# Performance work log

Measured on AMD Instinct MI355X. Metric: run time of the kernel, lower is better.

## Reference

```python
import jax, jax.numpy as jnp
import numpy as np

B, S, DIM = 2, 2048, 2048
H, HKV = 16, 8
HD = DIM // H          # 128
N_REP = H // HKV       # 2
EPS = 1e-6


def rmsnorm(x, w):
    return x * jax.lax.rsqrt(jnp.mean(x * x, axis=-1, keepdims=True) + EPS) * w


def apply_rope(x, cis):
    # x: [b, s, h, hd]; cis: [b, s, hd//2, 2] (cos, sin)
    xr = x.reshape(*x.shape[:-1], HD // 2, 2)
    x_re, x_im = xr[..., 0], xr[..., 1]
    c_re = cis[..., 0][:, :, None, :]  # broadcast over heads
    c_im = cis[..., 1][:, :, None, :]
    o_re = x_re * c_re - x_im * c_im
    o_im = x_re * c_im + x_im * c_re
    return jnp.stack([o_re, o_im], axis=-1).reshape(x.shape)


def setup_inputs() -> dict:
    key = jax.random.key(0)
    k1, k2, k3 = jax.random.split(key, 3)
    x = jax.random.normal(k1, (B, S, DIM), dtype=jnp.float32)
    x_mask = jnp.ones((B, S), dtype=bool)
    # rotary freqs: standard 10000-base, precomputed as (cos, sin)
    inv_freq = 1.0 / (10000.0 ** (jnp.arange(0, HD, 2, dtype=jnp.float32) / HD))
    ang = jnp.arange(S, dtype=jnp.float32)[:, None] * inv_freq[None, :]  # [s, hd//2]
    cis = jnp.stack([jnp.cos(ang), jnp.sin(ang)], axis=-1)               # [s, hd//2, 2]
    freqs_cis = jnp.broadcast_to(cis[None], (B, S, HD // 2, 2))
    scale = 1.0 / np.sqrt(DIM)
    w_qkv = jax.random.normal(k2, ((H + 2 * HKV) * HD, DIM), dtype=jnp.float32) * scale
    w_out = jax.random.normal(k3, (DIM, H * HD), dtype=jnp.float32) * scale
    q_norm_w = jnp.ones((HD,), dtype=jnp.float32)
    k_norm_w = jnp.ones((HD,), dtype=jnp.float32)
    return {"x": x, "x_mask": x_mask, "freqs_cis": freqs_cis,
            "w_qkv": w_qkv, "w_out": w_out,
            "q_norm_w": q_norm_w, "k_norm_w": k_norm_w}


def reference(x, x_mask, freqs_cis, w_qkv, w_out, q_norm_w, k_norm_w):
    bsz, seqlen, _ = x.shape
    qkv = x @ w_qkv.T                                   # [b, s, (H+2*HKV)*HD]
    xq, xk, xv = jnp.split(qkv, [H * HD, (H + HKV) * HD], axis=-1)
    xq = xq.reshape(bsz, seqlen, H, HD)
    xk = xk.reshape(bsz, seqlen, HKV, HD)
    xv = xv.reshape(bsz, seqlen, HKV, HD)
    xq = rmsnorm(xq, q_norm_w)
    xk = rmsnorm(xk, k_norm_w)
    xq = apply_rope(xq, freqs_cis)
    xk = apply_rope(xk, freqs_cis)
    # GQA: repeat kv heads (torch: unsqueeze/repeat/flatten)
    xk = jnp.repeat(xk, N_REP, axis=2)                  # [b, s, H, HD]
    xv = jnp.repeat(xv, N_REP, axis=2)
    softmax_scale = 1.0 / np.sqrt(HD)
    scores = jnp.einsum('bqhd,bkhd->bhqk', xq, xk) * softmax_scale
    scores = jnp.where(x_mask[:, None, None, :], scores, jnp.float32(-1e9))
    attn = jax.nn.softmax(scores, axis=-1)
    out = jnp.einsum('bhqk,bkhd->bqhd', attn, xv)       # [b, s, H, HD]
    out = out.reshape(bsz, seqlen, H * HD)
    return out @ w_out.T
```

## Files before the change

kernel.cpp:

```cpp
#include <hip/hip_runtime.h>


typedef __attribute__((ext_vector_type(8))) short short8;
typedef __attribute__((ext_vector_type(8))) unsigned short ushort8;
typedef __attribute__((ext_vector_type(4))) float f32x4;
typedef __attribute__((ext_vector_type(16))) float f32x16;

__device__ __forceinline__ unsigned short to_bf16(float f) {
  union { float f; unsigned u; } v; v.f = f;
  unsigned r = v.u + 0x7fffu + ((v.u >> 16) & 1u);
  return (unsigned short)(r >> 16);
}
__device__ __forceinline__ float bfhi_f32(unsigned u) {
  union { unsigned u; float f; } v; v.u = u & 0xffff0000u; return v.f;
}
__device__ __forceinline__ float bflo_f32(unsigned u) {
  union { unsigned u; float f; } v; v.u = u << 16; return v.f;
}

#define GLOAD16(gp, lp) __builtin_amdgcn_global_load_lds(                      \
    (const __attribute__((address_space(1))) void*)(gp),                       \
    (__attribute__((address_space(3))) void*)(lp), 16, 0, 0)

__global__ __launch_bounds__(256) void cvt3_bf16_k(const float* __restrict__ s0,
                                                   const float* __restrict__ s1,
                                                   const float* __restrict__ s2,
                                                   unsigned short* __restrict__ d0,
                                                   unsigned short* __restrict__ d1,
                                                   unsigned short* __restrict__ d2) {
  int i = blockIdx.x * 256 + threadIdx.x;
  const float* sp; unsigned short* dp;
  if (i < 1048576)      { sp = s0; dp = d0; }
  else if (i < 2097152) { sp = s1; dp = d1; i -= 1048576; }
  else                  { sp = s2; dp = d2; i -= 2097152; }
  const float4* v = (const float4*)sp + (size_t)i * 2;
  float4 a = v[0], b = v[1];
  ushort8 t;
  t[0] = to_bf16(a.x); t[1] = to_bf16(a.y); t[2] = to_bf16(a.z); t[3] = to_bf16(a.w);
  t[4] = to_bf16(b.x); t[5] = to_bf16(b.y); t[6] = to_bf16(b.z); t[7] = to_bf16(b.w);
  *((ushort8*)dp + i) = t;
}

#define SWZ(r, cb) ((cb) ^ (((r) & 7) << 4))

#define VMW_STEADY() do {                                                      \
    if constexpr (BM == 256) asm volatile("s_waitcnt vmcnt(6)" ::: "memory");  \
    else                     asm volatile("s_waitcnt vmcnt(5)" ::: "memory");  \
  } while (0)

#define STAGE_HALF(sb, sm, sh, skt) do {                                       \
    const char* gb_ = (sm) ? gB : gA;                                          \
    char* lb_ = ldsAB + (sb) * BUFSTR +                                        \
                ((sm) ? 2 * AH + (sh) * 16384 : (sh) * AH);                    \
    const int rows_ = (sm) ? 128 : (BM >> 1);                                  \
    const int nld_ = (sm) ? 2 : (BM >> 7);                                     \
    _Pragma("unroll")                                                          \
    for (int j_ = 0; j_ < nld_; ++j_) {                                        \
      const int c_ = tid + j_ * 512;                                           \
      const int rl_ = c_ >> 3, u_ = c_ & 7;                                    \
      GLOAD16(gb_ + (size_t)((sh) * rows_ + rl_) * rstr + (size_t)(skt) * 128  \
                  + SWZ(rl_, u_ * 16),                                         \
              lb_ + j_ * 8192 + wv * 1024);                                    \
    }                                                                          \
  } while (0)

#define GPHASE(bb, qd, sb, sm, sh, skt, DOVM) do {                             \
    _Pragma("unroll")                                                          \
    for (int i_ = 0; i_ < FPP; ++i_) {                                         \
      _Pragma("unroll")                                                        \
      for (int ks_ = 0; ks_ < 2; ++ks_) {                                      \
        const int ar_ = ((qd) * FPP + i_) * 16 + r15;                          \
        af[i_][ks_] = *(const short8*)(ldsAB + (bb) * BUFSTR + wr * AH         \
                        + ar_ * 128 + SWZ(ar_, ks_ * 64 + g4 * 16));           \
      }                                                                        \
    }                                                                          \
    if ((qd) == 0) {                                                           \
      _Pragma("unroll")                                                        \
      for (int ni_ = 0; ni_ < 4; ++ni_)                                        \
        _Pragma("unroll")                                                      \
        for (int ks_ = 0; ks_ < 2; ++ks_) {                                    \
          const int br_ = (wc & 1) * 64 + ni_ * 16 + r15;                      \
          bf[ni_][ks_] = *(const short8*)(ldsAB + (bb) * BUFSTR + 2 * AH       \
                           + (wc >> 1) * 16384 + br_ * 128                     \
                           + SWZ(br_, ks_ * 64 + g4 * 16));                    \
        }                                                                      \
    }                                                                          \
    asm volatile("s_waitcnt lgkmcnt(0)" ::: "memory");                         \
    __builtin_amdgcn_sched_barrier(0);                                         \
    STAGE_HALF(sb, sm, sh, skt);                                               \
    __builtin_amdgcn_s_barrier();                                              \
    __builtin_amdgcn_s_setprio(1);                                             \
    _Pragma("unroll")                                                          \
    for (int ni_ = 0; ni_ < 4; ++ni_)                                          \
      _Pragma("unroll")                                                        \
      for (int i_ = 0; i_ < FPP; ++i_)                                         \
        _Pragma("unroll")                                                      \
        for (int ks_ = 0; ks_ < 2; ++ks_)                                      \
          acc[(qd) * FPP + i_][ni_] = __builtin_amdgcn_mfma_f32_16x16x32_bf16( \
              af[i_][ks_], bf[ni_][ks_], acc[(qd) * FPP + i_][ni_], 0, 0, 0);  \
    __builtin_amdgcn_s_setprio(0);                                             \
    if (DOVM) VMW_STEADY();                                                    \
    __builtin_amdgcn_s_barrier();                                              \
  } while (0)

template <int BM, typename OT>
__global__ __launch_bounds__(512, 2) void gemm8p_k(const unsigned short* __restrict__ A,
                                                   const unsigned short* __restrict__ B,
                                                   OT* __restrict__ C,
                                                   int M, int N, int K) {
  constexpr int AH = BM * 64;
  constexpr int BUFSTR = 2 * AH + 32768;
  constexpr int FPP = BM / 128;
  constexpr int MFR = BM / 32;
  __shared__ __align__(16) char ldsAB[2 * BUFSTR];
  const int tid = threadIdx.x, lane = tid & 63, wv = tid >> 6;
  const int wr = wv >> 2, wc = wv & 3;
  const int r15 = lane & 15, g4 = lane >> 4;
  const int gx = gridDim.x, nwg = gx * gridDim.y;
  int bid = blockIdx.y * gx + blockIdx.x;
  bid = (bid & 7) * (nwg >> 3) + (bid >> 3);
  const int m0 = (bid / gx) * BM, n0 = (bid % gx) << 8;
  const char* gA = (const char*)(A + (size_t)m0 * K);
  const char* gB = (const char*)(B + (size_t)n0 * K);
  const size_t rstr = (size_t)K * 2;
  const int KT = K >> 6, NIT = KT >> 1;

  f32x4 acc[MFR][4];
  #pragma unroll
  for (int mi = 0; mi < MFR; ++mi)
    #pragma unroll
    for (int ni = 0; ni < 4; ++ni) acc[mi][ni] = (f32x4){0.f, 0.f, 0.f, 0.f};
  short8 af[2][2], bf[4][2];

  STAGE_HALF(0, 1, 0, 0); STAGE_HALF(0, 1, 1, 0);
  STAGE_HALF(0, 0, 0, 0); STAGE_HALF(0, 0, 1, 0);
  STAGE_HALF(1, 1, 0, 1); STAGE_HALF(1, 1, 1, 1);
  STAGE_HALF(1, 0, 0, 1);
  VMW_STEADY();
  __builtin_amdgcn_s_barrier();

  for (int it = 0; it < NIT; ++it) {
    const int kt1c = 2 * it + 1;
    int ktn0 = 2 * it + 2; if (ktn0 > KT - 1) ktn0 = KT - 1;
    int ktn1 = 2 * it + 3; if (ktn1 > KT - 1) ktn1 = KT - 1;
    GPHASE(0, 0, 1, 0, 1, kt1c, 0);
    GPHASE(0, 1, 0, 1, 0, ktn0, 0);
    GPHASE(0, 2, 0, 1, 1, ktn0, 0);
    GPHASE(0, 3, 0, 0, 0, ktn0, 1);
    GPHASE(1, 0, 0, 0, 1, ktn0, 0);
    GPHASE(1, 1, 1, 1, 0, ktn1, 0);
    GPHASE(1, 2, 1, 1, 1, ktn1, 0);
    GPHASE(1, 3, 1, 0, 0, ktn1, 1);
  }
  asm volatile("s_waitcnt vmcnt(0)" ::: "memory");

  const int crow = m0 + wr * (BM >> 1), ccol = n0 + wc * 64;
  #pragma unroll
  for (int mi = 0; mi < MFR; ++mi)
    #pragma unroll
    for (int ni = 0; ni < 4; ++ni)
      #pragma unroll
      for (int r = 0; r < 4; ++r) {
        const size_t idx = (size_t)(crow + mi * 16 + g4 * 4 + r) * N
                         + (ccol + ni * 16 + r15);
        if constexpr (sizeof(OT) == 4) C[idx] = acc[mi][ni][r];
        else                           C[idx] = to_bf16(acc[mi][ni][r]);
      }
}

__global__ __launch_bounds__(256) void rmsrope_k(const unsigned short* __restrict__ qkv,
                                                 const float* __restrict__ freqs,
                                                 const float* __restrict__ qw,
                                                 const float* __restrict__ kw,
                                                 unsigned short* __restrict__ Qg,
                                                 unsigned short* __restrict__ Kg) {
  const int row = blockIdx.x;
  const int b = row >> 11, s = row & 2047;
  const int lane = threadIdx.x & 63, wave = threadIdx.x >> 6;
  const unsigned short* base = qkv + (size_t)row * 4096;
  const float2 cs = ((const float2*)(freqs + (size_t)row * 128))[lane];
  const int tile = s >> 6, kv = s & 63;
  for (int hh = wave; hh < 24; hh += 4) {
    const bool isq = hh < 16;
    const unsigned u = *(const unsigned*)(base + hh * 128 + 2 * lane);
    const float xre = bflo_f32(u), xim = bfhi_f32(u);
    float ssq = xre * xre + xim * xim;
    #pragma unroll
    for (int m = 1; m <= 32; m <<= 1) ssq += __shfl_xor(ssq, m);
    const float rs = rsqrtf(ssq * (1.0f / 128.0f) + 1e-6f);
    const float sscale = isq ? 0.12751743f : 1.0f;
    const float* wp = isq ? qw : kw;
    const float xr = xre * rs * wp[2 * lane];
    const float xi = xim * rs * wp[2 * lane + 1];
    const float o_re = (xr * cs.x - xi * cs.y) * sscale;
    const float o_im = (xr * cs.y + xi * cs.x) * sscale;
    unsigned pk = (unsigned)to_bf16(o_re) | ((unsigned)to_bf16(o_im) << 16);
    if (isq) {
      *(unsigned*)(Qg + ((size_t)(b * 16 + hh) * 2048 + s) * 128 + 2 * lane) = pk;
    } else {
      const int kvh = b * 8 + (hh - 16);
      const size_t off = ((size_t)(kvh * 32 + tile) * 16 + (lane >> 2)) * 1024
                       + kv * 16 + (lane & 3) * 4;
      *(unsigned*)((char*)Kg + off) = pk;
    }
  }
}

__global__ __launch_bounds__(128) void transpose_v_k(const unsigned short* __restrict__ qkv,
                                                     unsigned short* __restrict__ Vt) {
  const int sc = blockIdx.x, bh = blockIdx.y;
  const int b = bh >> 3, d = threadIdx.x, s0 = sc << 6;
  const unsigned short* src = qkv + (size_t)(b * 2048 + s0) * 4096
                              + (3072 + (bh & 7) * 128 + d);
  char* dstT = (char*)Vt + (size_t)(bh * 32 + sc) * 16384;
  for (int j0 = 0; j0 < 64; j0 += 8) {
    ushort8 t;
    #pragma unroll
    for (int j = 0; j < 8; ++j) t[j] = src[(size_t)(j0 + j) * 4096];
    *(ushort8*)(dstT + (((j0 >> 3) * 128 + d) << 4)) = t;
  }
}

__global__ __launch_bounds__(512, 1) void attn32_k(const unsigned short* __restrict__ Qg,
                                                   const unsigned short* __restrict__ Kg,
                                                   const unsigned short* __restrict__ Vt,
                                                   unsigned short* __restrict__ Og) {
  __shared__ __align__(16) unsigned short Ks[3][64 * 128];
  __shared__ __align__(16) unsigned short Vs[3][128 * 64];
  const int tid = threadIdx.x, lane = tid & 63, wv = tid >> 6;
  const int l31 = lane & 31, hi = lane >> 5;
  const int bh = blockIdx.y, b = bh >> 4, h = bh & 15;
  const int kvh = b * 8 + (h >> 1);
  const int qw = (blockIdx.x << 8) + wv * 32;
  const char* Qbase = (const char*)(Qg + ((size_t)bh * 2048 + qw) * 128);
  const char* Kbase = (const char*)Kg + (size_t)kvh * 524288;
  const char* Vbase = (const char*)Vt + (size_t)kvh * 524288;
  const int kox = hi * 1024 + l31 * 16;
  const int vox = hi * 2048 + l31 * 16;

  short8 qf[8];
  #pragma unroll
  for (int kk = 0; kk < 8; ++kk)
    qf[kk] = *(const short8*)(Qbase + l31 * 256 + kk * 32 + hi * 16);

  f32x16 oa[4];
  #pragma unroll
  for (int d = 0; d < 4; ++d)
    #pragma unroll
    for (int r = 0; r < 16; ++r) oa[d][r] = 0.f;
  float m2 = 0.f, lrun = 0.f;

#define STAGE_KV(tt, bb) do {                                                  \
    const char* ks_ = Kbase + (size_t)(tt) * 16384;                            \
    const char* vs_ = Vbase + (size_t)(tt) * 16384;                            \
    _Pragma("unroll")                                                          \
    for (int i_ = 0; i_ < 2; ++i_) {                                           \
      const int c_ = (i_ * 512 + tid) << 4;                                    \
      GLOAD16(ks_ + c_, (char*)Ks[bb] + c_);                                   \
      GLOAD16(vs_ + c_, (char*)Vs[bb] + c_);                                   \
    }                                                                          \
  } while (0)

  STAGE_KV(0, 0);
  STAGE_KV(1, 1);
  asm volatile("s_waitcnt vmcnt(4)" ::: "memory");
  __builtin_amdgcn_sched_barrier(0);
  __builtin_amdgcn_s_barrier();
  __builtin_amdgcn_sched_barrier(0);

  int c0 = 0, c1 = 1, c2 = 2;
  for (int t = 0; t < 32; ++t) {
    if (t < 30) STAGE_KV(t + 2, c2);
    const char* KsB = (const char*)Ks[0] + c0 * 16384;
    const char* VsB = (const char*)Vs[0] + c0 * 16384;

    f32x16 sc[2];
    #pragma unroll
    for (int c = 0; c < 2; ++c)
      #pragma unroll
      for (int r = 0; r < 16; ++r) sc[c][r] = 0.f;
    __builtin_amdgcn_s_setprio(1);
    #pragma unroll
    for (int kk = 0; kk < 8; ++kk) {
      #pragma unroll
      for (int c = 0; c < 2; ++c) {
        short8 kf = *(const short8*)(KsB + kk * 2048 + c * 512 + kox);
        sc[c] = __builtin_amdgcn_mfma_f32_32x32x16_bf16(kf, qf[kk], sc[c], 0, 0, 0);
      }
    }
    __builtin_amdgcn_s_setprio(0);

    float p0[16], p1[16];
    #pragma unroll
    for (int r = 0; r < 16; ++r) p0[r] = __builtin_amdgcn_exp2f(sc[0][r] - m2);
    #pragma unroll
    for (int r = 0; r < 16; ++r) p1[r] = __builtin_amdgcn_exp2f(sc[1][r] - m2);
    float tm[8];
    #pragma unroll
    for (int r = 0; r < 8; ++r)
      tm[r] = fmaxf(fmaxf(p0[r], p0[r + 8]), fmaxf(p1[r], p1[r + 8]));
    #pragma unroll
    for (int s = 4; s; s >>= 1)
      #pragma unroll
      for (int r = 0; r < s; ++r) tm[r] = fmaxf(tm[r], tm[r + s]);
    const float pmax = fmaxf(tm[0], __shfl_xor(tm[0], 32));
    if (!__all(pmax <= 256.f)) {
      float sm[8];
      #pragma unroll
      for (int r = 0; r < 8; ++r)
        sm[r] = fmaxf(fmaxf(sc[0][r], sc[0][r + 8]),
                      fmaxf(sc[1][r], sc[1][r + 8]));
      #pragma unroll
      for (int s = 4; s; s >>= 1)
        #pragma unroll
        for (int r = 0; r < s; ++r) sm[r] = fmaxf(sm[r], sm[r + s]);
      float smax = fmaxf(sm[0], __shfl_xor(sm[0], 32));
      smax = fmaxf(smax, m2);
      const float al = __builtin_amdgcn_exp2f(m2 - smax);
      lrun *= al;
      #pragma unroll
      for (int r = 0; r < 16; ++r) {
        const int crr = (r & 3) + ((r >> 2) << 3) + (hi << 2);
        const float aq = __shfl(al, crr);
        #pragma unroll
        for (int d = 0; d < 4; ++d) oa[d][r] *= aq;
      }
      m2 = smax;
      #pragma unroll
      for (int r = 0; r < 16; ++r) p0[r] = __builtin_amdgcn_exp2f(sc[0][r] - m2);
      #pragma unroll
      for (int r = 0; r < 16; ++r) p1[r] = __builtin_amdgcn_exp2f(sc[1][r] - m2);
    }
    float ts[8];
    #pragma unroll
    for (int r = 0; r < 8; ++r)
      ts[r] = (p0[r] + p0[r + 8]) + (p1[r] + p1[r + 8]);
    #pragma unroll
    for (int s = 4; s; s >>= 1)
      #pragma unroll
      for (int r = 0; r < s; ++r) ts[r] += ts[r + s];
    lrun += ts[0];

    short8 pa[4];
    #pragma unroll
    for (int ks = 0; ks < 4; ++ks) {
      const int base = (ks & 1) << 3;
      const float* pp = (ks >> 1) ? p1 : p0;
      unsigned w0, w1, w2, w3;
      asm("v_cvt_pk_bf16_f32 %0, %1, %2" : "=v"(w0)
          : "v"(pp[base + 0]), "v"(pp[base + 1]));
      asm("v_cvt_pk_bf16_f32 %0, %1, %2" : "=v"(w1)
          : "v"(pp[base + 2]), "v"(pp[base + 3]));
      asm("v_cvt_pk_bf16_f32 %0, %1, %2" : "=v"(w2)
          : "v"(pp[base + 4]), "v"(pp[base + 5]));
      asm("v_cvt_pk_bf16_f32 %0, %1, %2" : "=v"(w3)
          : "v"(pp[base + 6]), "v"(pp[base + 7]));
      asm("v_permlane32_swap_b32 %0, %1" : "+v"(w0), "+v"(w2));
      asm("v_permlane32_swap_b32 %0, %1" : "+v"(w1), "+v"(w3));
      union { unsigned u[4]; short8 s8; } pu;
      pu.u[0] = w0; pu.u[1] = w1; pu.u[2] = w2; pu.u[3] = w3;
      pa[ks] = pu.s8;
    }

    __builtin_amdgcn_s_setprio(1);
    #pragma unroll
    for (int ks = 0; ks < 4; ++ks) {
      #pragma unroll
      for (int d = 0; d < 4; ++d) {
        short8 vf = *(const short8*)(VsB + ks * 4096 + d * 512 + vox);
        oa[d] = __builtin_amdgcn_mfma_f32_32x32x16_bf16(pa[ks], vf, oa[d], 0, 0, 0);
      }
    }
    __builtin_amdgcn_s_setprio(0);

    __builtin_amdgcn_sched_barrier(0);
    if (t < 30) asm volatile("s_waitcnt vmcnt(4)" ::: "memory");
    else        asm volatile("s_waitcnt vmcnt(0)" ::: "memory");
    asm volatile("s_waitcnt lgkmcnt(0)" ::: "memory");
    __builtin_amdgcn_sched_barrier(0);
    __builtin_amdgcn_s_barrier();
    __builtin_amdgcn_sched_barrier(0);
    { const int tp = c0; c0 = c1; c1 = c2; c2 = tp; }
  }

  const float lt = lrun + __shfl_xor(lrun, 32);
  const float inv = 1.f / lt;
  #pragma unroll
  for (int r = 0; r < 16; ++r) {
    const int crr = (r & 3) + ((r >> 2) << 3) + (hi << 2);
    const float iv = __shfl(inv, crr);
    const size_t rowoff = (size_t)(b * 2048 + qw + crr) * 2048 + h * 128;
    #pragma unroll
    for (int d = 0; d < 4; ++d)
      Og[rowoff + d * 32 + l31] = to_bf16(oa[d][r] * iv);
  }
}

extern "C" void kernel_launch(void* const* d_in, const int* in_sizes, int n_in,
                              void* d_out, int out_size, void* d_ws, size_t ws_size,
                              hipStream_t stream) {
  const float* x     = (const float*)d_in[0];
  const float* freqs = (const float*)d_in[2];
  const float* w_qkv = (const float*)d_in[3];
  const float* w_out = (const float*)d_in[4];
  const float* qnw   = (const float*)d_in[5];
  const float* knw   = (const float*)d_in[6];
  float* out = (float*)d_out;

  char* ws = (char*)d_ws;
  unsigned short* x_bf    = (unsigned short*)(ws);
  unsigned short* wqkv_bf = (unsigned short*)(ws + (16u << 20));
  unsigned short* wout_bf = (unsigned short*)(ws + (32u << 20));
  unsigned short* qkvb    = (unsigned short*)(ws + (40u << 20));
  unsigned short* Qg      = (unsigned short*)(ws + (104u << 20));
  unsigned short* Kg      = (unsigned short*)(ws + (120u << 20));
  unsigned short* Vt       = wqkv_bf;
  unsigned short* attn_out = x_bf;

  cvt3_bf16_k<<<10240, 256, 0, stream>>>(x, w_qkv, w_out, x_bf, wqkv_bf, wout_bf);
  gemm8p_k<256, unsigned short><<<dim3(16, 16), 512, 0, stream>>>(
      x_bf, wqkv_bf, qkvb, 4096, 4096, 2048);
  rmsrope_k<<<4096, 256, 0, stream>>>(qkvb, freqs, qnw, knw, Qg, Kg);
  transpose_v_k<<<dim3(32, 16), 128, 0, stream>>>(qkvb, Vt);
  attn32_k<<<dim3(8, 32), 512, 0, stream>>>(Qg, Kg, Vt, attn_out);
  gemm8p_k<128, float><<<dim3(8, 32), 512, 0, stream>>>(
      attn_out, wout_bf, out, 4096, 2048, 2048);
}
```

Baseline: 211.9 us.

## Process KV tiles in pairs with double buffering, halving barriers per pass

The attention loop now stages two 64-key KV tiles per iteration into a double-buffered LDS layout, replacing the triple-buffered single-tile ring. Each iteration runs both QK^T products up front, then softmax and PV for each tile in turn. This halves the number of block barriers and waits, and gives the scheduler more independent MFMA work. In exchange it prefetches only one pair ahead, drops the setprio hints, uses more LDS (128KB) and more registers, and the wait is now vmcnt(0) every iteration.

Result: faster. 207.0 us (-2.3%).

```diff
diff --git a/kernel.cpp b/kernel.cpp
--- a/kernel.cpp
+++ b/kernel.cpp
@@ -225,8 +225,8 @@
                                                    const unsigned short* __restrict__ Kg,
                                                    const unsigned short* __restrict__ Vt,
                                                    unsigned short* __restrict__ Og) {
-  __shared__ __align__(16) unsigned short Ks[3][64 * 128];
-  __shared__ __align__(16) unsigned short Vs[3][128 * 64];
+  __shared__ __align__(16) char KsL[2 * 32768];
+  __shared__ __align__(16) char VsL[2 * 32768];
   const int tid = threadIdx.x, lane = tid & 63, wv = tid >> 6;
   const int l31 = lane & 31, hi = lane >> 5;
   const int bh = blockIdx.y, b = bh >> 4, h = bh & 15;
@@ -250,137 +250,148 @@
     for (int r = 0; r < 16; ++r) oa[d][r] = 0.f;
   float m2 = 0.f, lrun = 0.f;
 
-#define STAGE_KV(tt, bb) do {                                                  \
-    const char* ks_ = Kbase + (size_t)(tt) * 16384;                            \
-    const char* vs_ = Vbase + (size_t)(tt) * 16384;                            \
+#define STAGE_PAIR(tp, pb) do {                                                \
+    const char* kp_ = Kbase + (size_t)(tp) * 32768;                            \
+    const char* vp_ = Vbase + (size_t)(tp) * 32768;                            \
     _Pragma("unroll")                                                          \
     for (int i_ = 0; i_ < 2; ++i_) {                                           \
       const int c_ = (i_ * 512 + tid) << 4;                                    \
-      GLOAD16(ks_ + c_, (char*)Ks[bb] + c_);                                   \
-      GLOAD16(vs_ + c_, (char*)Vs[bb] + c_);                                   \
-    }                                                                          \
-  } while (0)
-
-  STAGE_KV(0, 0);
-  STAGE_KV(1, 1);
-  asm volatile("s_waitcnt vmcnt(4)" ::: "memory");
+      GLOAD16(kp_ + c_,         KsL + (pb) * 32768 + c_);                      \
+      GLOAD16(kp_ + 16384 + c_, KsL + (pb) * 32768 + 16384 + c_);              \
+      GLOAD16(vp_ + c_,         VsL + (pb) * 32768 + c_);                      \
+      GLOAD16(vp_ + 16384 + c_, VsL + (pb) * 32768 + 16384 + c_);              \
+    }                                                                          \
+  } while (0)
+
+#define QK_TILE(scv, ksb) do {                                                 \
+    _Pragma("unroll")                                                          \
+    for (int c = 0; c < 2; ++c)                                                \
+      _Pragma("unroll")                                                        \
+      for (int r = 0; r < 16; ++r) scv[c][r] = 0.f;                            \
+    _Pragma("unroll")                                                          \
+    for (int kk = 0; kk < 8; ++kk) {                                           \
+      _Pragma("unroll")                                                        \
+      for (int c = 0; c < 2; ++c) {                                            \
+        short8 kf = *(const short8*)((ksb) + kk * 2048 + c * 512 + kox);       \
+        scv[c] = __builtin_amdgcn_mfma_f32_32x32x16_bf16(kf, qf[kk], scv[c],   \
+                                                         0, 0, 0);             \
+      }                                                                        \
+    }                                                                          \
+  } while (0)
+
+#define SM_TILE(scv, pp0, pp1) do {                                            \
+    _Pragma("unroll")                                                          \
+    for (int r = 0; r < 16; ++r) pp0[r] = __builtin_amdgcn_exp2f(scv[0][r] - m2); \
+    _Pragma("unroll")                                                          \
+    for (int r = 0; r < 16; ++r) pp1[r] = __builtin_amdgcn_exp2f(scv[1][r] - m2); \
+    float tm[8];                                                               \
+    _Pragma("unroll")                                                          \
+    for (int r = 0; r < 8; ++r)                                                \
+      tm[r] = fmaxf(fmaxf(pp0[r], pp0[r + 8]), fmaxf(pp1[r], pp1[r + 8]));     \
+    _Pragma("unroll")                                                          \
+    for (int s = 4; s; s >>= 1)                                                \
+      _Pragma("unroll")                                                        \
+      for (int r = 0; r < s; ++r) tm[r] = fmaxf(tm[r], tm[r + s]);             \
+    const float pmax = fmaxf(tm[0], __shfl_xor(tm[0], 32));                    \
+    if (!__all(pmax <= 256.f)) {                             \
+      float sm_[8];                                                            \
+      _Pragma("unroll")                                                        \
+      for (int r = 0; r < 8; ++r)                                              \
+        sm_[r] = fmaxf(fmaxf(scv[0][r], scv[0][r + 8]),                        \
+                       fmaxf(scv[1][r], scv[1][r + 8]));                       \
+      _Pragma("unroll")                                                        \
+      for (int s = 4; s; s >>= 1)                                              \
+        _Pragma("unroll")                                                      \
+        for (int r = 0; r < s; ++r) sm_[r] = fmaxf(sm_[r], sm_[r + s]);        \
+      float smax = fmaxf(sm_[0], __shfl_xor(sm_[0], 32));                      \
+      smax = fmaxf(smax, m2);                                                  \
+      const float al = __builtin_amdgcn_exp2f(m2 - smax);                      \
+      lrun *= al;                                                              \
+      _Pragma("unroll")                                                        \
+      for (int r = 0; r < 16; ++r) {                                           \
+        const int crr = (r & 3) + ((r >> 2) << 3) + (hi << 2);                 \
+        const float aq = __shfl(al, crr);                                      \
+        _Pragma("unroll")                                                      \
+        for (int d = 0; d < 4; ++d) oa[d][r] *= aq;                            \
+      }                                                                        \
+      m2 = smax;                                                               \
+      _Pragma("unroll")                                                        \
+      for (int r = 0; r < 16; ++r) pp0[r] = __builtin_amdgcn_exp2f(scv[0][r] - m2); \
+      _Pragma("unroll")                                                        \
+      for (int r = 0; r < 16; ++r) pp1[r] = __builtin_amdgcn_exp2f(scv[1][r] - m2); \
+    }                                                                          \
+    float ts[8];                                                               \
+    _Pragma("unroll")                                                          \
+    for (int r = 0; r < 8; ++r)                                                \
+      ts[r] = (pp0[r] + pp0[r + 8]) + (pp1[r] + pp1[r + 8]);                   \
+    _Pragma("unroll")                                                          \
+    for (int s = 4; s; s >>= 1)                                                \
+      _Pragma("unroll")                                                        \
+      for (int r = 0; r < s; ++r) ts[r] += ts[r + s];                          \
+    lrun += ts[0];                                                             \
+  } while (0)
+
+#define PV_TILE(pp0, pp1, vsb) do {                                            \
+    short8 pa[4];                                                              \
+    _Pragma("unroll")                                                          \
+    for (int ks = 0; ks < 4; ++ks) {                                           \
+      const int base = (ks & 1) << 3;                                          \
+      const float* pp = (ks >> 1) ? pp1 : pp0;                                 \
+      unsigned w0, w1, w2, w3;                                                 \
+      asm("v_cvt_pk_bf16_f32 %0, %1, %2" : "=v"(w0)                            \
+          : "v"(pp[base + 0]), "v"(pp[base + 1]));                             \
+      asm("v_cvt_pk_bf16_f32 %0, %1, %2" : "=v"(w1)                            \
+          : "v"(pp[base + 2]), "v"(pp[base + 3]));                             \
+      asm("v_cvt_pk_bf16_f32 %0, %1, %2" : "=v"(w2)                            \
+          : "v"(pp[base + 4]), "v"(pp[base + 5]));                             \
+      asm("v_cvt_pk_bf16_f32 %0, %1, %2" : "=v"(w3)                            \
+          : "v"(pp[base + 6]), "v"(pp[base + 7]));                             \
+      asm("v_permlane32_swap_b32 %0, %1" : "+v"(w0), "+v"(w2));                \
+      asm("v_permlane32_swap_b32 %0, %1" : "+v"(w1), "+v"(w3));                \
+      union { unsigned u[4]; short8 s8; } pu;                                  \
+      pu.u[0] = w0; pu.u[1] = w1; pu.u[2] = w2; pu.u[3] = w3;                  \
+      pa[ks] = pu.s8;                                                          \
+    }                                                                          \
+    _Pragma("unroll")                                                          \
+    for (int ks = 0; ks < 4; ++ks) {                                           \
+      _Pragma("unroll")                                                        \
+      for (int d = 0; d < 4; ++d) {                                            \
+        short8 vf = *(const short8*)((vsb) + ks * 4096 + d * 512 + vox);       \
+        oa[d] = __builtin_amdgcn_mfma_f32_32x32x16_bf16(pa[ks], vf, oa[d],     \
+                                                        0, 0, 0);              \
+      }                                                                        \
+    }                                                                          \
+  } while (0)
+
+  STAGE_PAIR(0, 0);
+  asm volatile("s_waitcnt vmcnt(0)" ::: "memory");
   __builtin_amdgcn_sched_barrier(0);
   __builtin_amdgcn_s_barrier();
   __builtin_amdgcn_sched_barrier(0);
 
-  int c0 = 0, c1 = 1, c2 = 2;
-  for (int t = 0; t < 32; ++t) {
-    if (t < 30) STAGE_KV(t + 2, c2);
-    const char* KsB = (const char*)Ks[0] + c0 * 16384;
-    const char* VsB = (const char*)Vs[0] + c0 * 16384;
-
-    f32x16 sc[2];
-    #pragma unroll
-    for (int c = 0; c < 2; ++c)
-      #pragma unroll
-      for (int r = 0; r < 16; ++r) sc[c][r] = 0.f;
-    __builtin_amdgcn_s_setprio(1);
-    #pragma unroll
-    for (int kk = 0; kk < 8; ++kk) {
-      #pragma unroll
-      for (int c = 0; c < 2; ++c) {
-        short8 kf = *(const short8*)(KsB + kk * 2048 + c * 512 + kox);
-        sc[c] = __builtin_amdgcn_mfma_f32_32x32x16_bf16(kf, qf[kk], sc[c], 0, 0, 0);
-      }
-    }
-    __builtin_amdgcn_s_setprio(0);
-
-    float p0[16], p1[16];
-    #pragma unroll
-    for (int r = 0; r < 16; ++r) p0[r] = __builtin_amdgcn_exp2f(sc[0][r] - m2);
-    #pragma unroll
-    for (int r = 0; r < 16; ++r) p1[r] = __builtin_amdgcn_exp2f(sc[1][r] - m2);
-    float tm[8];
-    #pragma unroll
-    for (int r = 0; r < 8; ++r)
-      tm[r] = fmaxf(fmaxf(p0[r], p0[r + 8]), fmaxf(p1[r], p1[r + 8]));
-    #pragma unroll
-    for (int s = 4; s; s >>= 1)
-      #pragma unroll
-      for (int r = 0; r < s; ++r) tm[r] = fmaxf(tm[r], tm[r + s]);
-    const float pmax = fmaxf(tm[0], __shfl_xor(tm[0], 32));
-    if (!__all(pmax <= 256.f)) {
-      float sm[8];
-      #pragma unroll
-      for (int r = 0; r < 8; ++r)
-        sm[r] = fmaxf(fmaxf(sc[0][r], sc[0][r + 8]),
-                      fmaxf(sc[1][r], sc[1][r + 8]));
-      #pragma unroll
-      for (int s = 4; s; s >>= 1)
-        #pragma unroll
-        for (int r = 0; r < s; ++r) sm[r] = fmaxf(sm[r], sm[r + s]);
-      float smax = fmaxf(sm[0], __shfl_xor(sm[0], 32));
-      smax = fmaxf(smax, m2);
-      const float al = __builtin_amdgcn_exp2f(m2 - smax);
-      lrun *= al;
-      #pragma unroll
-      for (int r = 0; r < 16; ++r) {
-        const int crr = (r & 3) + ((r >> 2) << 3) + (hi << 2);
-        const float aq = __shfl(al, crr);
-        #pragma unroll
-        for (int d = 0; d < 4; ++d) oa[d][r] *= aq;
-      }
-      m2 = smax;
-      #pragma unroll
-      for (int r = 0; r < 16; ++r) p0[r] = __builtin_amdgcn_exp2f(sc[0][r] - m2);
-      #pragma unroll
-      for (int r = 0; r < 16; ++r) p1[r] = __builtin_amdgcn_exp2f(sc[1][r] - m2);
-    }
-    float ts[8];
-    #pragma unroll
-    for (int r = 0; r < 8; ++r)
-      ts[r] = (p0[r] + p0[r + 8]) + (p1[r] + p1[r + 8]);
-    #pragma unroll
-    for (int s = 4; s; s >>= 1)
-      #pragma unroll
-      for (int r = 0; r < s; ++r) ts[r] += ts[r + s];
-    lrun += ts[0];
-
-    short8 pa[4];
-    #pragma unroll
-    for (int ks = 0; ks < 4; ++ks) {
-      const int base = (ks & 1) << 3;
-      const float* pp = (ks >> 1) ? p1 : p0;
-      unsigned w0, w1, w2, w3;
-      asm("v_cvt_pk_bf16_f32 %0, %1, %2" : "=v"(w0)
-          : "v"(pp[base + 0]), "v"(pp[base + 1]));
-      asm("v_cvt_pk_bf16_f32 %0, %1, %2" : "=v"(w1)
-          : "v"(pp[base + 2]), "v"(pp[base + 3]));
-      asm("v_cvt_pk_bf16_f32 %0, %1, %2" : "=v"(w2)
-          : "v"(pp[base + 4]), "v"(pp[base + 5]));
-      asm("v_cvt_pk_bf16_f32 %0, %1, %2" : "=v"(w3)
-          : "v"(pp[base + 6]), "v"(pp[base + 7]));
-      asm("v_permlane32_swap_b32 %0, %1" : "+v"(w0), "+v"(w2));
-      asm("v_permlane32_swap_b32 %0, %1" : "+v"(w1), "+v"(w3));
-      union { unsigned u[4]; short8 s8; } pu;
-      pu.u[0] = w0; pu.u[1] = w1; pu.u[2] = w2; pu.u[3] = w3;
-      pa[ks] = pu.s8;
-    }
-
-    __builtin_amdgcn_s_setprio(1);
-    #pragma unroll
-    for (int ks = 0; ks < 4; ++ks) {
-      #pragma unroll
-      for (int d = 0; d < 4; ++d) {
-        short8 vf = *(const short8*)(VsB + ks * 4096 + d * 512 + vox);
-        oa[d] = __builtin_amdgcn_mfma_f32_32x32x16_bf16(pa[ks], vf, oa[d], 0, 0, 0);
-      }
-    }
-    __builtin_amdgcn_s_setprio(0);
+  for (int t = 0; t < 16; ++t) {
+    const int pb = t & 1;
+    if (t < 15) STAGE_PAIR(t + 1, pb ^ 1);
+    const char* Ka = KsL + pb * 32768;
+    const char* Kb = Ka + 16384;
+    const char* Va = VsL + pb * 32768;
+    const char* Vb = Va + 16384;
+
+    f32x16 sca[2], scb[2];
+    float p0a[16], p1a[16], p0b[16], p1b[16];
+    QK_TILE(sca, Ka);
+    QK_TILE(scb, Kb);
+    SM_TILE(sca, p0a, p1a);
+    PV_TILE(p0a, p1a, Va);
+    SM_TILE(scb, p0b, p1b);
+    PV_TILE(p0b, p1b, Vb);
 
     __builtin_amdgcn_sched_barrier(0);
-    if (t < 30) asm volatile("s_waitcnt vmcnt(4)" ::: "memory");
-    else        asm volatile("s_waitcnt vmcnt(0)" ::: "memory");
+    asm volatile("s_waitcnt vmcnt(0)" ::: "memory");
     asm volatile("s_waitcnt lgkmcnt(0)" ::: "memory");
     __builtin_amdgcn_sched_barrier(0);
     __builtin_amdgcn_s_barrier();
     __builtin_amdgcn_sched_barrier(0);
-    { const int tp = c0; c0 = c1; c1 = c2; c2 = tp; }
   }
 
   const float lt = lrun + __shfl_xor(lrun, 32);
```
